# Kernel tuning notes

Hardware: AMD Instinct MI355X
Metric: run time of the kernel (lower is better)

The kernel has to match this reference:

```python
import jax, jax.numpy as jnp
import numpy as np

N, E, G = 50000, 1000000, 8
H, C, L = 4, 32, 3          # heads, per-head channels, GAT layers
HID = H * C                  # 128
NODE_D, EDGE_D, REC_D = 64, 16, 8
NEG_SLOPE = 0.2              # PyG GATConv default


def setup_inputs() -> dict:
    key = jax.random.key(0)
    ks = jax.random.split(key, 24)

    def glorot(k, shape):
        fan_in = shape[-2] if len(shape) >= 2 else shape[-1]
        return jax.random.normal(k, shape, dtype=jnp.float32) / jnp.sqrt(jnp.float32(fan_in))

    inp = {
        "x": jax.random.normal(ks[0], (N, NODE_D), dtype=jnp.float32),
        "edge_index": jax.random.randint(ks[1], (2, E), 0, N, dtype=jnp.int64),
        "edge_attr": jax.random.normal(ks[2], (E, EDGE_D), dtype=jnp.float32),
        "batch": jnp.sort(jax.random.randint(ks[3], (N,), 0, G, dtype=jnp.int64)),
        "recipe": jax.random.normal(ks[4], (G, REC_D), dtype=jnp.float32),
        # input projection + edge encoder
        "W_in": glorot(ks[5], (NODE_D + REC_D, HID)),
        "b_in": jnp.zeros((HID,), jnp.float32),
        "W_edge": glorot(ks[6], (EDGE_D, HID)),
        "b_edge": jnp.zeros((HID,), jnp.float32),
        # stacked GATConv params (PyG GATConv: lin & lin_edge have no bias)
        "lin_w": glorot(ks[7], (L, HID, HID)),
        "lin_edge_w": glorot(ks[8], (L, HID, HID)),
        "att_src": glorot(ks[9], (L, H, C)),
        "att_dst": glorot(ks[10], (L, H, C)),
        "att_edge": glorot(ks[11], (L, H, C)),
        "gat_bias": jnp.zeros((L, HID), jnp.float32),
        "W1": glorot(ks[12], (HID, HID)),
        "b1": jnp.zeros((HID,), jnp.float32),
        "W2": glorot(ks[13], (HID, 1)),
        "b2": jnp.zeros((1,), jnp.float32),
    }
    return inp


def reference(x, edge_index, edge_attr, batch, recipe,
              W_in, b_in, W_edge, b_edge,
              lin_w, lin_edge_w, att_src, att_dst, att_edge, gat_bias,
              W1, b1, W2, b2):
    src, dst = edge_index[0], edge_index[1]

    # broadcast recipe to nodes, project, relu
    h = jnp.concatenate([x, recipe[batch]], axis=1)        # [N, NODE_D+REC_D]
    h = jax.nn.relu(h @ W_in + b_in)                        # [N, HID]
    e = edge_attr @ W_edge + b_edge                         # [E, HID]

    for l in range(L):
        xl = (h @ lin_w[l]).reshape(N, H, C)                # [N,H,C]
        el = (e @ lin_edge_w[l]).reshape(E, H, C)           # [E,H,C]
        a_src = jnp.sum(xl * att_src[l], axis=-1)           # [N,H]
        a_dst = jnp.sum(xl * att_dst[l], axis=-1)           # [N,H]
        a_edge = jnp.sum(el * att_edge[l], axis=-1)         # [E,H]
        alpha = jax.nn.leaky_relu(a_src[src] + a_dst[dst] + a_edge, NEG_SLOPE)
        # segment softmax over destination nodes
        amax = jax.ops.segment_max(alpha, dst, num_segments=N)   # [N,H]
        alpha = jnp.exp(alpha - amax[dst])
        denom = jax.ops.segment_sum(alpha, dst, num_segments=N)  # [N,H]
        alpha = alpha / denom[dst]
        # weighted message scatter-add (dropout is identity in eval mode)
        msg = xl[src] * alpha[..., None]                    # [E,H,C]
        out = jax.ops.segment_sum(msg, dst, num_segments=N).reshape(N, HID) + gat_bias[l]
        h = jax.nn.relu(out)

    # global mean pool over graphs
    counts = jax.ops.segment_sum(jnp.ones((N,), h.dtype), batch, num_segments=G)
    g = jax.ops.segment_sum(h, batch, num_segments=G) / jnp.maximum(counts, 1.0)[:, None]

    return jax.nn.relu(g @ W1 + b1) @ W2 + b2               # [G,1]
```

## Files before the change

kernel.cpp:

```cpp
#include <hip/hip_runtime.h>
#include <math.h>


typedef __attribute__((ext_vector_type(8))) __bf16 bf16x8;
typedef __attribute__((ext_vector_type(4))) float f32x4;

union FragU {
  uint4 u;
  bf16x8 v;
};

__device__ __forceinline__ float lrelu(float x) { return x >= 0.f ? x : 0.2f * x; }

__device__ __forceinline__ unsigned pack_bf2(float a, float b) {
  unsigned ua = __float_as_uint(a), ub = __float_as_uint(b);
  ua += 0x7fffu + ((ua >> 16) & 1u);
  ub += 0x7fffu + ((ub >> 16) & 1u);
  return (ua >> 16) | (ub & 0xffff0000u);
}
__device__ __forceinline__ unsigned short bf_of(float a) {
  unsigned ua = __float_as_uint(a);
  ua += 0x7fffu + ((ua >> 16) & 1u);
  return (unsigned short)(ua >> 16);
}
__device__ __forceinline__ float bf_lo(unsigned u) { return __uint_as_float(u << 16); }
__device__ __forceinline__ float bf_hi(unsigned u) { return __uint_as_float(u & 0xffff0000u); }

__global__ void rank_kernel(const int* __restrict__ dst, int* __restrict__ deg,
                            int* __restrict__ rank, int E) {
  int e = blockIdx.x * 256 + threadIdx.x;
  if (e < E) rank[e] = atomicAdd(&deg[dst[e]], 1);
}

__global__ __launch_bounds__(1024) void scanA_kernel(const int* __restrict__ deg,
                                                     int* __restrict__ tmp,
                                                     int* __restrict__ bsum, int n) {
  __shared__ int wsum[16];
  int tid = threadIdx.x;
  int lane = tid & 63, wid = tid >> 6;
  int i = blockIdx.x * 1024 + tid;
  int v = (i < n) ? deg[i] : 0;
  int sv = v;
#pragma unroll
  for (int off = 1; off < 64; off <<= 1) {
    int t = __shfl_up(sv, off);
    if (lane >= off) sv += t;
  }
  if (lane == 63) wsum[wid] = sv;
  __syncthreads();
  if (wid == 0) {
    int wv = (lane < 16) ? wsum[lane] : 0;
#pragma unroll
    for (int off = 1; off < 16; off <<= 1) {
      int t = __shfl_up(wv, off);
      if (lane >= off) wv += t;
    }
    if (lane < 16) wsum[lane] = wv;
  }
  __syncthreads();
  int waveoff = (wid > 0) ? wsum[wid - 1] : 0;
  int incl = waveoff + sv;
  if (i < n) tmp[i] = incl;
  if (tid == 1023) bsum[blockIdx.x] = incl;
}

__global__ void scanB_kernel(int* __restrict__ bsum, int nb, int* __restrict__ total_out) {
  int lane = threadIdx.x;
  int v = (lane < nb) ? bsum[lane] : 0;
  int sv = v;
#pragma unroll
  for (int off = 1; off < 64; off <<= 1) {
    int t = __shfl_up(sv, off);
    if (lane >= off) sv += t;
  }
  if (lane < nb) bsum[lane] = sv - v;
  if (lane == 63) *total_out = sv;
}

__global__ __launch_bounds__(1024) void scanC_kernel(const int* __restrict__ deg,
                                                     const int* __restrict__ tmp,
                                                     const int* __restrict__ bsum,
                                                     int* __restrict__ row_ptr, int n) {
  int i = blockIdx.x * 1024 + threadIdx.x;
  if (i < n) row_ptr[i] = tmp[i] - deg[i] + bsum[blockIdx.x];
}

__global__ void perm_kernel(const int* __restrict__ dst, const int* __restrict__ srcA,
                            const int* __restrict__ rank, const int* __restrict__ row_ptr,
                            int* __restrict__ perm, int* __restrict__ src_csr, int E) {
  int e = blockIdx.x * 256 + threadIdx.x;
  if (e < E) {
    int pos = row_ptr[dst[e]] + rank[e];
    perm[pos] = e;
    src_csr[pos] = srcA[e];
  }
}

__global__ void gb_kernel(const int* __restrict__ batch, int* __restrict__ gb, int N) {
  int i = blockIdx.x * 256 + threadIdx.x;
  if (i == 0) gb[8] = N;
  if (i < N) {
    int b = batch[i];
    if (i == 0 || batch[i - 1] != b) gb[b] = i;
  }
}

__global__ void prep_params(const float* __restrict__ lin_edge_w,
                            const float* __restrict__ att_edge,
                            const float* __restrict__ W_edge,
                            const float* __restrict__ b_edge,
                            float* __restrict__ Mc) {
  __shared__ float WE[128][12];
  int t = threadIdx.x;
  for (int idx = t; idx < 128 * 12; idx += 256) {
    int k = idx / 12, j = idx - k * 12;
    int l = j >> 2, h = j & 3;
    float s = 0.f;
    for (int c = 0; c < 32; ++c)
      s += lin_edge_w[((size_t)l * 128 + k) * 128 + h * 32 + c] * att_edge[(l * 4 + h) * 32 + c];
    WE[k][j] = s;
  }
  __syncthreads();
  for (int idx = t; idx < 16 * 12; idx += 256) {
    int i = idx / 12, j = idx - i * 12;
    float s = 0.f;
    for (int k = 0; k < 128; ++k) s += W_edge[i * 128 + k] * WE[k][j];
    Mc[idx] = s;
  }
  if (t < 12) {
    float s = 0.f;
    for (int k = 0; k < 128; ++k) s += b_edge[k] * WE[k][t];
    Mc[192 + t] = s;
  }
}

__global__ __launch_bounds__(256) void prep_w_kernel(const float* __restrict__ lin_w,
                                                     unsigned short* __restrict__ wt_hi,
                                                     unsigned short* __restrict__ wt_lo) {
  __shared__ float tile[128][18];
  int l = blockIdx.x >> 3;
  int n0 = (blockIdx.x & 7) * 16;
  const float* W = lin_w + (size_t)l * 16384;
  unsigned short* hi = wt_hi + (size_t)l * 16384;
  unsigned short* lo = wt_lo + (size_t)l * 16384;
  int t = threadIdx.x;
  for (int idx = t; idx < 2048; idx += 256) {
    int k = idx >> 4, j = idx & 15;
    tile[k][j] = W[k * 128 + n0 + j];
  }
  __syncthreads();
  int r = t >> 4;
  int k0 = (t & 15) * 8;
  unsigned short hbuf[8], lbuf[8];
#pragma unroll
  for (int u = 0; u < 8; ++u) {
    float w = tile[k0 + u][r];
    unsigned short hb = bf_of(w);
    float hf = __uint_as_float((unsigned)hb << 16);
    hbuf[u] = hb;
    lbuf[u] = bf_of(w - hf);
  }
  size_t base = (size_t)(n0 + r) * 128 + k0;
  *(uint4*)(hi + base) = *(uint4*)hbuf;
  *(uint4*)(lo + base) = *(uint4*)lbuf;
}

__global__ void edge_build_kernel(const int* __restrict__ perm,
                                  const float* __restrict__ edge_attr,
                                  const float* __restrict__ Mc,
                                  unsigned short* __restrict__ a_edge_csr,
                                  int E) {
  __shared__ float M[16][12];
  __shared__ float cv[12];
  int t = threadIdx.x;
  if (t < 192) M[t / 12][t % 12] = Mc[t];
  if (t < 12) cv[t] = Mc[192 + t];
  __syncthreads();
  int i = blockIdx.x * 256 + t;
  if (i >= E) return;
  int e = perm[i];
  const float4* p = (const float4*)(edge_attr + (size_t)e * 16);
  float4 v0 = p[0], v1 = p[1], v2 = p[2], v3 = p[3];
  float ea[16] = {v0.x, v0.y, v0.z, v0.w, v1.x, v1.y, v1.z, v1.w,
                  v2.x, v2.y, v2.z, v2.w, v3.x, v3.y, v3.z, v3.w};
  float a[12];
#pragma unroll
  for (int j = 0; j < 12; ++j) {
    float s = cv[j];
#pragma unroll
    for (int k = 0; k < 16; ++k) s += ea[k] * M[k][j];
    a[j] = s;
  }
#pragma unroll
  for (int l = 0; l < 3; ++l) {
    uint2 o;
    o.x = pack_bf2(a[l * 4 + 0], a[l * 4 + 1]);
    o.y = pack_bf2(a[l * 4 + 2], a[l * 4 + 3]);
    *(uint2*)(a_edge_csr + ((size_t)l * E + i) * 4) = o;
  }
}

__global__ __launch_bounds__(256) void proj_kernel(const float* __restrict__ x,
                                                   const float* __restrict__ recipe,
                                                   const int* __restrict__ batch,
                                                   const float* __restrict__ W_in,
                                                   const float* __restrict__ b_in,
                                                   float* __restrict__ h, int N) {
  __shared__ float Wc[72][128];
  __shared__ float Ac[64][72];
  int t = threadIdx.x;
  int tx = t & 31, ty = t >> 5;
  int row0 = blockIdx.x * 64;
  for (int idx = t; idx < 2304; idx += 256) {
    int k = idx >> 5, c4 = idx & 31;
    *(float4*)&Wc[k][c4 * 4] = *(const float4*)(W_in + (size_t)k * 128 + c4 * 4);
  }
  for (int idx = t; idx < 1024; idx += 256) {
    int r = idx >> 4, c4 = idx & 15;
    int row = row0 + r;
    float4 v = make_float4(0.f, 0.f, 0.f, 0.f);
    if (row < N) v = *(const float4*)(x + (size_t)row * 64 + c4 * 4);
    *(float4*)&Ac[r][c4 * 4] = v;
  }
  for (int idx = t; idx < 128; idx += 256) {
    int r = idx >> 1, c4 = idx & 1;
    int row = row0 + r;
    float4 v = make_float4(0.f, 0.f, 0.f, 0.f);
    if (row < N) v = *(const float4*)(recipe + (size_t)batch[row] * 8 + c4 * 4);
    *(float4*)&Ac[r][64 + c4 * 4] = v;
  }
  __syncthreads();
  float4 bias = *(const float4*)(b_in + tx * 4);
  float4 acc[8];
#pragma unroll
  for (int s = 0; s < 8; ++s) acc[s] = bias;
  for (int k4 = 0; k4 < 18; ++k4) {
    float4 w0 = *(float4*)&Wc[k4 * 4 + 0][tx * 4];
    float4 w1 = *(float4*)&Wc[k4 * 4 + 1][tx * 4];
    float4 w2 = *(float4*)&Wc[k4 * 4 + 2][tx * 4];
    float4 w3 = *(float4*)&Wc[k4 * 4 + 3][tx * 4];
#pragma unroll
    for (int s = 0; s < 8; ++s) {
      float4 av = *(float4*)&Ac[ty + 8 * s][k4 * 4];
      acc[s].x += av.x * w0.x + av.y * w1.x + av.z * w2.x + av.w * w3.x;
      acc[s].y += av.x * w0.y + av.y * w1.y + av.z * w2.y + av.w * w3.y;
      acc[s].z += av.x * w0.z + av.y * w1.z + av.z * w2.z + av.w * w3.z;
      acc[s].w += av.x * w0.w + av.y * w1.w + av.z * w2.w + av.w * w3.w;
    }
  }
#pragma unroll
  for (int s = 0; s < 8; ++s) {
    int row = row0 + ty + 8 * s;
    if (row < N) {
      float4 o = acc[s];
      o.x = fmaxf(o.x, 0.f); o.y = fmaxf(o.y, 0.f);
      o.z = fmaxf(o.z, 0.f); o.w = fmaxf(o.w, 0.f);
      *(float4*)(h + (size_t)row * 128 + tx * 4) = o;
    }
  }
}

__global__ __launch_bounds__(256) void gemm_mfma_kernel(
    const float* __restrict__ A, const unsigned short* __restrict__ wt_hi,
    const unsigned short* __restrict__ wt_lo,
    const float* __restrict__ att_s, const float* __restrict__ att_d,
    unsigned short* __restrict__ Cb, float* __restrict__ a_src,
    float* __restrict__ a_dst, int M) {
  int t = threadIdx.x;
  int lane = t & 63, w = t >> 6;
  int c = lane & 15, q = lane >> 4;
  int m0 = blockIdx.x * 64 + w * 16;
  int rowA = m0 + c;
  bool rowok = rowA < M;

  f32x4 acc[8];
#pragma unroll
  for (int n = 0; n < 8; ++n) acc[n] = 0.f;

#pragma unroll
  for (int kk = 0; kk < 128; kk += 32) {
    float4 fa0 = make_float4(0.f, 0.f, 0.f, 0.f), fa1 = fa0;
    if (rowok) {
      const float* ap = A + (size_t)rowA * 128 + kk + 8 * q;
      fa0 = *(const float4*)ap;
      fa1 = *(const float4*)(ap + 4);
    }
    FragU af;
    af.u.x = pack_bf2(fa0.x, fa0.y);
    af.u.y = pack_bf2(fa0.z, fa0.w);
    af.u.z = pack_bf2(fa1.x, fa1.y);
    af.u.w = pack_bf2(fa1.z, fa1.w);
    const unsigned short* bhp = wt_hi + (size_t)c * 128 + kk + 8 * q;
    const unsigned short* blp = wt_lo + (size_t)c * 128 + kk + 8 * q;
#pragma unroll
    for (int n = 0; n < 8; ++n) {
      FragU bh, bl;
      bh.u = *(const uint4*)(bhp + n * 2048);
      bl.u = *(const uint4*)(blp + n * 2048);
      acc[n] = __builtin_amdgcn_mfma_f32_16x16x32_bf16(af.v, bh.v, acc[n], 0, 0, 0);
      acc[n] = __builtin_amdgcn_mfma_f32_16x16x32_bf16(af.v, bl.v, acc[n], 0, 0, 0);
    }
  }

  float asr[4][2], adr[4][2];
#pragma unroll
  for (int hh = 0; hh < 4; ++hh) {
    asr[hh][0] = att_s[32 * hh + c];
    asr[hh][1] = att_s[32 * hh + 16 + c];
    adr[hh][0] = att_d[32 * hh + c];
    adr[hh][1] = att_d[32 * hh + 16 + c];
  }
#pragma unroll
  for (int i = 0; i < 4; ++i) {
    int row = m0 + 4 * q + i;
    bool ok = row < M;
    if (ok) {
      size_t base = (size_t)row * 128;
#pragma unroll
      for (int n = 0; n < 8; ++n) Cb[base + n * 16 + c] = bf_of(acc[n][i]);
    }
#pragma unroll
    for (int hh = 0; hh < 4; ++hh) {
      float ps = acc[2 * hh][i] * asr[hh][0] + acc[2 * hh + 1][i] * asr[hh][1];
      float pd = acc[2 * hh][i] * adr[hh][0] + acc[2 * hh + 1][i] * adr[hh][1];
#pragma unroll
      for (int off = 1; off < 16; off <<= 1) {
        ps += __shfl_xor(ps, off);
        pd += __shfl_xor(pd, off);
      }
      if (ok && c == hh) {
        a_src[(size_t)row * 4 + hh] = ps;
        a_dst[(size_t)row * 4 + hh] = pd;
      }
    }
  }
}

__global__ __launch_bounds__(256) void node_kernel(const int* __restrict__ row_ptr,
                                                   const int* __restrict__ src_csr,
                                                   const float* __restrict__ a_src,
                                                   const float* __restrict__ a_dst,
                                                   const unsigned short* __restrict__ aep,
                                                   const unsigned short* __restrict__ xlb,
                                                   const float* __restrict__ bias,
                                                   float* __restrict__ h_out, int N) {
  int lane = threadIdx.x & 63;
  int g = lane >> 3;
  int t = lane & 7;
  int h = t >> 1;
  int n = blockIdx.x * 4 + (threadIdx.x >> 6);
  if (n >= N) return;
  int s = row_ptr[n], e = row_ptr[n + 1];

  const float* bp = bias + t * 16;
  float* op = h_out + (size_t)n * 128 + t * 16;
  if (e <= s) {
    if (g == 0) {
#pragma unroll
      for (int q = 0; q < 4; ++q) {
        float4 b = *(const float4*)(bp + q * 4);
        float4 o = make_float4(fmaxf(b.x, 0.f), fmaxf(b.y, 0.f), fmaxf(b.z, 0.f), fmaxf(b.w, 0.f));
        *(float4*)(op + q * 4) = o;
      }
    }
    return;
  }

  float ad = a_dst[(size_t)n * 4 + h];
  const unsigned* aepu = (const unsigned*)aep;
  int hw = h >> 1;
  int hb = h & 1;

  float den = 0.f;
  float num[16];
#pragma unroll
  for (int c = 0; c < 16; ++c) num[c] = 0.f;

  for (int i = s + g; i < e; i += 8) {
    int sc = src_csr[i];
    float as = a_src[(size_t)sc * 4 + h];
    unsigned uae = aepu[(size_t)i * 2 + hw];
    float ae = hb ? bf_hi(uae) : bf_lo(uae);
    const uint4* xp = (const uint4*)(xlb + (size_t)sc * 128 + t * 16);
    uint4 u0 = xp[0], u1 = xp[1];
    float a = lrelu(as + ad + ae);
    float w = __expf(fminf(a, 80.f));
    den += w;
    num[0]  += w * bf_lo(u0.x); num[1]  += w * bf_hi(u0.x);
    num[2]  += w * bf_lo(u0.y); num[3]  += w * bf_hi(u0.y);
    num[4]  += w * bf_lo(u0.z); num[5]  += w * bf_hi(u0.z);
    num[6]  += w * bf_lo(u0.w); num[7]  += w * bf_hi(u0.w);
    num[8]  += w * bf_lo(u1.x); num[9]  += w * bf_hi(u1.x);
    num[10] += w * bf_lo(u1.y); num[11] += w * bf_hi(u1.y);
    num[12] += w * bf_lo(u1.z); num[13] += w * bf_hi(u1.z);
    num[14] += w * bf_lo(u1.w); num[15] += w * bf_hi(u1.w);
  }

#pragma unroll
  for (int off = 8; off < 64; off <<= 1) {
    den += __shfl_xor(den, off);
#pragma unroll
    for (int c = 0; c < 16; ++c) num[c] += __shfl_xor(num[c], off);
  }

  if (g == 0) {
    float rh = 1.f / den;
#pragma unroll
    for (int q = 0; q < 4; ++q) {
      float4 b = *(const float4*)(bp + q * 4);
      float4 o;
      o.x = fmaxf(num[q * 4 + 0] * rh + b.x, 0.f);
      o.y = fmaxf(num[q * 4 + 1] * rh + b.y, 0.f);
      o.z = fmaxf(num[q * 4 + 2] * rh + b.z, 0.f);
      o.w = fmaxf(num[q * 4 + 3] * rh + b.w, 0.f);
      *(float4*)(op + q * 4) = o;
    }
  }
}

__global__ __launch_bounds__(256) void pool_kernel(const float* __restrict__ h,
                                                   const int* __restrict__ gb,
                                                   float* __restrict__ g_sum, int N) {
  __shared__ int st[9];
  __shared__ float red[8][132];
  int t = threadIdx.x;
  if (t < 9) {
    int m = 0x7fffffff;
    for (int j = t; j < 9; ++j) m = min(m, gb[j]);
    st[t] = min(m, N);
  }
  __syncthreads();
  int g = blockIdx.x >> 5;
  int chunk = blockIdx.x & 31;
  int gs = st[g], ge = st[g + 1];
  int rows = ge - gs;
  int c4 = t & 31, sub = t >> 5;
  float ax = 0.f, ay = 0.f, az = 0.f, aw = 0.f;
  if (rows > 0) {
    int clen = (rows + 31) >> 5;
    int cs = gs + chunk * clen;
    int ce = min(cs + clen, ge);
    for (int r = cs + sub; r < ce; r += 8) {
      float4 v = *(const float4*)(h + (size_t)r * 128 + c4 * 4);
      ax += v.x; ay += v.y; az += v.z; aw += v.w;
    }
  }
  red[sub][c4 * 4 + 0] = ax;
  red[sub][c4 * 4 + 1] = ay;
  red[sub][c4 * 4 + 2] = az;
  red[sub][c4 * 4 + 3] = aw;
  __syncthreads();
  if (t < 128 && rows > 0) {
    float s = 0.f;
#pragma unroll
    for (int u = 0; u < 8; ++u) s += red[u][t];
    atomicAdd(&g_sum[(size_t)g * 128 + t], s);
  }
}

__global__ void head_kernel(const float* __restrict__ g_sum, const int* __restrict__ gb,
                            const float* __restrict__ W1, const float* __restrict__ b1,
                            const float* __restrict__ W2, const float* __restrict__ b2,
                            float* __restrict__ out, int N) {
  __shared__ float g[8][128];
  __shared__ float t1[8][128];
  __shared__ int st[9];
  int t = threadIdx.x;
  if (t < 9) {
    int m = 0x7fffffff;
    for (int j = t; j < 9; ++j) m = min(m, gb[j]);
    st[t] = min(m, N);
  }
  __syncthreads();
  for (int idx = t; idx < 1024; idx += 256) {
    int gi = idx >> 7, ch = idx & 127;
    float cnt = (float)(st[gi + 1] - st[gi]);
    g[gi][ch] = g_sum[idx] / fmaxf(cnt, 1.f);
  }
  __syncthreads();
  for (int idx = t; idx < 1024; idx += 256) {
    int gi = idx >> 7, j = idx & 127;
    float a = b1[j];
    for (int k = 0; k < 128; ++k) a += g[gi][k] * W1[(size_t)k * 128 + j];
    t1[gi][j] = fmaxf(a, 0.f);
  }
  __syncthreads();
  if (t < 8) {
    float a = b2[0];
    for (int j = 0; j < 128; ++j) a += t1[t][j] * W2[j];
    out[t] = a;
  }
}

extern "C" void kernel_launch(void* const* d_in, const int* in_sizes, int n_in,
                              void* d_out, int out_size, void* d_ws, size_t ws_size,
                              hipStream_t stream) {
  const float* x         = (const float*)d_in[0];
  const int*   edge_idx  = (const int*)d_in[1];
  const float* edge_attr = (const float*)d_in[2];
  const int*   batch     = (const int*)d_in[3];
  const float* recipe    = (const float*)d_in[4];
  const float* W_in      = (const float*)d_in[5];
  const float* b_in      = (const float*)d_in[6];
  const float* W_edge    = (const float*)d_in[7];
  const float* b_edge    = (const float*)d_in[8];
  const float* lin_w     = (const float*)d_in[9];
  const float* lin_edge_w= (const float*)d_in[10];
  const float* att_src   = (const float*)d_in[11];
  const float* att_dst   = (const float*)d_in[12];
  const float* att_edge  = (const float*)d_in[13];
  const float* gat_bias  = (const float*)d_in[14];
  const float* W1        = (const float*)d_in[15];
  const float* b1        = (const float*)d_in[16];
  const float* W2        = (const float*)d_in[17];
  const float* b2p       = (const float*)d_in[18];

  const int N = in_sizes[3];
  const int E = in_sizes[1] / 2;
  const int* src = edge_idx;
  const int* dst = edge_idx + E;

  char* ws = (char*)d_ws;
  size_t off = 0;
  auto alloc = [&](size_t bytes) -> void* {
    void* p = ws + off;
    off += (bytes + 255) & ~(size_t)255;
    return p;
  };
  float* hA         = (float*)alloc((size_t)N * 128 * 4);
  float* hB         = (float*)alloc((size_t)N * 128 * 4);
  unsigned short* xlb = (unsigned short*)alloc((size_t)N * 128 * 2);
  float* a_srcA     = (float*)alloc((size_t)N * 4 * 4);
  float* a_dstA     = (float*)alloc((size_t)N * 4 * 4);
  unsigned short* a_edge_csr = (unsigned short*)alloc((size_t)3 * E * 4 * 2);
  int*   src_csr    = (int*)alloc((size_t)E * 4);
  int*   rank       = (int*)alloc((size_t)E * 4);
  int*   perm       = (int*)alloc((size_t)E * 4);
  int*   row_ptr    = (int*)alloc((size_t)(N + 1) * 4);
  int*   deg        = (int*)alloc((size_t)N * 4);
  int*   scan_tmp   = (int*)alloc((size_t)N * 4);
  int*   bsum       = (int*)alloc(64 * 4);
  float* Mc         = (float*)alloc(204 * 4);
  unsigned short* wt_hi = (unsigned short*)alloc((size_t)3 * 16384 * 2);
  unsigned short* wt_lo = (unsigned short*)alloc((size_t)3 * 16384 * 2);
  float* g_sum      = (float*)alloc(8 * 128 * 4);
  int*   gb         = (int*)alloc(9 * 4);
  (void)ws_size; (void)n_in; (void)out_size;

  const int eb = (E + 255) / 256;
  const int rowtiles = (N + 63) / 64;
  const int nb = (N + 1023) / 1024;

  hipMemsetAsync(deg, 0, (size_t)N * 4, stream);
  hipMemsetAsync(g_sum, 0, 8 * 128 * 4, stream);
  hipMemsetAsync(gb, 0x7f, 9 * 4, stream);

  rank_kernel<<<eb, 256, 0, stream>>>(dst, deg, rank, E);
  scanA_kernel<<<nb, 1024, 0, stream>>>(deg, scan_tmp, bsum, N);
  scanB_kernel<<<1, 64, 0, stream>>>(bsum, nb, row_ptr + N);
  scanC_kernel<<<nb, 1024, 0, stream>>>(deg, scan_tmp, bsum, row_ptr, N);
  perm_kernel<<<eb, 256, 0, stream>>>(dst, src, rank, row_ptr, perm, src_csr, E);
  gb_kernel<<<(N + 255) / 256, 256, 0, stream>>>(batch, gb, N);
  prep_params<<<1, 256, 0, stream>>>(lin_edge_w, att_edge, W_edge, b_edge, Mc);
  prep_w_kernel<<<24, 256, 0, stream>>>(lin_w, wt_hi, wt_lo);
  edge_build_kernel<<<eb, 256, 0, stream>>>(perm, edge_attr, Mc, a_edge_csr, E);
  proj_kernel<<<rowtiles, 256, 0, stream>>>(x, recipe, batch, W_in, b_in, hA, N);

  float* hcur = hA;
  float* hnxt = hB;
  for (int l = 0; l < 3; ++l) {
    gemm_mfma_kernel<<<rowtiles, 256, 0, stream>>>(hcur,
                                                   wt_hi + (size_t)l * 16384,
                                                   wt_lo + (size_t)l * 16384,
                                                   att_src + (size_t)l * 128,
                                                   att_dst + (size_t)l * 128,
                                                   xlb, a_srcA, a_dstA, N);
    node_kernel<<<(N + 3) / 4, 256, 0, stream>>>(row_ptr, src_csr, a_srcA, a_dstA,
                                                 a_edge_csr + (size_t)l * E * 4, xlb,
                                                 gat_bias + (size_t)l * 128, hnxt, N);
    float* tmp = hcur; hcur = hnxt; hnxt = tmp;
  }

  pool_kernel<<<256, 256, 0, stream>>>(hcur, gb, g_sum, N);
  head_kernel<<<1, 256, 0, stream>>>(g_sum, gb, W1, b1, W2, b2p, (float*)d_out, N);
}
```

Before: 448.3 us.

## Merge small setup kernels, pad degree counters, use bf16 union conversion

Folds the tiny scanB and gb kernels into scanA/scanC, and merges the two parameter-prep kernels into one launch, cutting the number of kernel launches. Pads each per-node degree counter to its own 64-byte slot so the atomics in rank_kernel no longer contend on shared cache lines, at the cost of a 16x larger memset and strided reads in the scan. The node kernel's bf16 unpacking is rewritten as a loop over a union of __bf16 values and left to the compiler, which may emit different conversion code.

```diff
diff --git a/kernel.cpp b/kernel.cpp
--- a/kernel.cpp
+++ b/kernel.cpp
@@ -8,6 +8,11 @@
 union FragU {
   uint4 u;
   bf16x8 v;
+};
+
+union XU {
+  uint4 u[2];
+  __bf16 b[16];
 };
 
 __device__ __forceinline__ float lrelu(float x) { return x >= 0.f ? x : 0.2f * x; }
@@ -29,17 +34,24 @@
 __global__ void rank_kernel(const int* __restrict__ dst, int* __restrict__ deg,
                             int* __restrict__ rank, int E) {
   int e = blockIdx.x * 256 + threadIdx.x;
-  if (e < E) rank[e] = atomicAdd(&deg[dst[e]], 1);
+  if (e < E) rank[e] = atomicAdd(&deg[(size_t)dst[e] * 16], 1);
 }
 
 __global__ __launch_bounds__(1024) void scanA_kernel(const int* __restrict__ deg,
+                                                     const int* __restrict__ batch,
                                                      int* __restrict__ tmp,
-                                                     int* __restrict__ bsum, int n) {
+                                                     int* __restrict__ bsum,
+                                                     int* __restrict__ gb, int n) {
   __shared__ int wsum[16];
   int tid = threadIdx.x;
   int lane = tid & 63, wid = tid >> 6;
   int i = blockIdx.x * 1024 + tid;
-  int v = (i < n) ? deg[i] : 0;
+  if (i == 0) gb[8] = n;
+  if (i < n) {
+    int b = batch[i];
+    if (i == 0 || batch[i - 1] != b) gb[b] = i;
+  }
+  int v = (i < n) ? deg[(size_t)i * 16] : 0;
   int sv = v;
 #pragma unroll
   for (int off = 1; off < 64; off <<= 1) {
@@ -64,25 +76,27 @@
   if (tid == 1023) bsum[blockIdx.x] = incl;
 }
 
-__global__ void scanB_kernel(int* __restrict__ bsum, int nb, int* __restrict__ total_out) {
-  int lane = threadIdx.x;
-  int v = (lane < nb) ? bsum[lane] : 0;
-  int sv = v;
-#pragma unroll
-  for (int off = 1; off < 64; off <<= 1) {
-    int t = __shfl_up(sv, off);
-    if (lane >= off) sv += t;
-  }
-  if (lane < nb) bsum[lane] = sv - v;
-  if (lane == 63) *total_out = sv;
-}
-
 __global__ __launch_bounds__(1024) void scanC_kernel(const int* __restrict__ deg,
                                                      const int* __restrict__ tmp,
-                                                     const int* __restrict__ bsum,
+                                                     const int* __restrict__ bsum, int nb,
                                                      int* __restrict__ row_ptr, int n) {
-  int i = blockIdx.x * 1024 + threadIdx.x;
-  if (i < n) row_ptr[i] = tmp[i] - deg[i] + bsum[blockIdx.x];
+  __shared__ int soff[2];
+  int tid = threadIdx.x;
+  if (tid < 64) {
+    int v = (tid < nb) ? bsum[tid] : 0;
+    int sv = v;
+#pragma unroll
+    for (int off = 1; off < 64; off <<= 1) {
+      int t = __shfl_up(sv, off);
+      if (tid >= off) sv += t;
+    }
+    if (tid == blockIdx.x) soff[0] = sv - v;
+    if (tid == 63) soff[1] = sv;
+  }
+  __syncthreads();
+  int i = blockIdx.x * 1024 + tid;
+  if (i < n) row_ptr[i] = tmp[i] - deg[(size_t)i * 16] + soff[0];
+  if (blockIdx.x == 0 && tid == 0) row_ptr[n] = soff[1];
 }
 
 __global__ void perm_kernel(const int* __restrict__ dst, const int* __restrict__ srcA,
@@ -96,73 +110,65 @@
   }
 }
 
-__global__ void gb_kernel(const int* __restrict__ batch, int* __restrict__ gb, int N) {
-  int i = blockIdx.x * 256 + threadIdx.x;
-  if (i == 0) gb[8] = N;
-  if (i < N) {
-    int b = batch[i];
-    if (i == 0 || batch[i - 1] != b) gb[b] = i;
-  }
-}
-
-__global__ void prep_params(const float* __restrict__ lin_edge_w,
-                            const float* __restrict__ att_edge,
-                            const float* __restrict__ W_edge,
-                            const float* __restrict__ b_edge,
-                            float* __restrict__ Mc) {
-  __shared__ float WE[128][12];
+__global__ __launch_bounds__(256) void prep_wp_kernel(const float* __restrict__ lin_w,
+                                                      unsigned short* __restrict__ wt_hi,
+                                                      unsigned short* __restrict__ wt_lo,
+                                                      const float* __restrict__ lin_edge_w,
+                                                      const float* __restrict__ att_edge,
+                                                      const float* __restrict__ W_edge,
+                                                      const float* __restrict__ b_edge,
+                                                      float* __restrict__ Mc) {
+  __shared__ float shmem[128 * 18];
   int t = threadIdx.x;
-  for (int idx = t; idx < 128 * 12; idx += 256) {
-    int k = idx / 12, j = idx - k * 12;
-    int l = j >> 2, h = j & 3;
-    float s = 0.f;
-    for (int c = 0; c < 32; ++c)
-      s += lin_edge_w[((size_t)l * 128 + k) * 128 + h * 32 + c] * att_edge[(l * 4 + h) * 32 + c];
-    WE[k][j] = s;
-  }
-  __syncthreads();
-  for (int idx = t; idx < 16 * 12; idx += 256) {
-    int i = idx / 12, j = idx - i * 12;
-    float s = 0.f;
-    for (int k = 0; k < 128; ++k) s += W_edge[i * 128 + k] * WE[k][j];
-    Mc[idx] = s;
-  }
-  if (t < 12) {
-    float s = 0.f;
-    for (int k = 0; k < 128; ++k) s += b_edge[k] * WE[k][t];
-    Mc[192 + t] = s;
-  }
-}
-
-__global__ __launch_bounds__(256) void prep_w_kernel(const float* __restrict__ lin_w,
-                                                     unsigned short* __restrict__ wt_hi,
-                                                     unsigned short* __restrict__ wt_lo) {
-  __shared__ float tile[128][18];
-  int l = blockIdx.x >> 3;
-  int n0 = (blockIdx.x & 7) * 16;
-  const float* W = lin_w + (size_t)l * 16384;
-  unsigned short* hi = wt_hi + (size_t)l * 16384;
-  unsigned short* lo = wt_lo + (size_t)l * 16384;
-  int t = threadIdx.x;
-  for (int idx = t; idx < 2048; idx += 256) {
-    int k = idx >> 4, j = idx & 15;
-    tile[k][j] = W[k * 128 + n0 + j];
-  }
-  __syncthreads();
-  int r = t >> 4;
-  int k0 = (t & 15) * 8;
-  unsigned short hbuf[8], lbuf[8];
-#pragma unroll
-  for (int u = 0; u < 8; ++u) {
-    float w = tile[k0 + u][r];
-    unsigned short hb = bf_of(w);
-    float hf = __uint_as_float((unsigned)hb << 16);
-    hbuf[u] = hb;
-    lbuf[u] = bf_of(w - hf);
-  }
-  size_t base = (size_t)(n0 + r) * 128 + k0;
-  *(uint4*)(hi + base) = *(uint4*)hbuf;
-  *(uint4*)(lo + base) = *(uint4*)lbuf;
+  if (blockIdx.x < 24) {
+    float(*tile)[18] = (float(*)[18])shmem;
+    int l = blockIdx.x >> 3;
+    int n0 = (blockIdx.x & 7) * 16;
+    const float* W = lin_w + (size_t)l * 16384;
+    unsigned short* hi = wt_hi + (size_t)l * 16384;
+    unsigned short* lo = wt_lo + (size_t)l * 16384;
+    for (int idx = t; idx < 2048; idx += 256) {
+      int k = idx >> 4, j = idx & 15;
+      tile[k][j] = W[k * 128 + n0 + j];
+    }
+    __syncthreads();
+    int r = t >> 4;
+    int k0 = (t & 15) * 8;
+    unsigned short hbuf[8], lbuf[8];
+#pragma unroll
+    for (int u = 0; u < 8; ++u) {
+      float w = tile[k0 + u][r];
+      unsigned short hb = bf_of(w);
+      float hf = __uint_as_float((unsigned)hb << 16);
+      hbuf[u] = hb;
+      lbuf[u] = bf_of(w - hf);
+    }
+    size_t base = (size_t)(n0 + r) * 128 + k0;
+    *(uint4*)(hi + base) = *(uint4*)hbuf;
+    *(uint4*)(lo + base) = *(uint4*)lbuf;
+  } else {
+    float(*WE)[12] = (float(*)[12])shmem;
+    for (int idx = t; idx < 128 * 12; idx += 256) {
+      int k = idx / 12, j = idx - k * 12;
+      int l = j >> 2, h = j & 3;
+      float s = 0.f;
+      for (int c = 0; c < 32; ++c)
+        s += lin_edge_w[((size_t)l * 128 + k) * 128 + h * 32 + c] * att_edge[(l * 4 + h) * 32 + c];
+      WE[k][j] = s;
+    }
+    __syncthreads();
+    for (int idx = t; idx < 16 * 12; idx += 256) {
+      int i = idx / 12, j = idx - i * 12;
+      float s = 0.f;
+      for (int k = 0; k < 128; ++k) s += W_edge[i * 128 + k] * WE[k][j];
+      Mc[idx] = s;
+    }
+    if (t < 12) {
+      float s = 0.f;
+      for (int k = 0; k < 128; ++k) s += b_edge[k] * WE[k][t];
+      Mc[192 + t] = s;
+    }
+  }
 }
 
 __global__ void edge_build_kernel(const int* __restrict__ perm,
@@ -382,18 +388,14 @@
     unsigned uae = aepu[(size_t)i * 2 + hw];
     float ae = hb ? bf_hi(uae) : bf_lo(uae);
     const uint4* xp = (const uint4*)(xlb + (size_t)sc * 128 + t * 16);
-    uint4 u0 = xp[0], u1 = xp[1];
+    XU xu;
+    xu.u[0] = xp[0];
+    xu.u[1] = xp[1];
     float a = lrelu(as + ad + ae);
     float w = __expf(fminf(a, 80.f));
     den += w;
-    num[0]  += w * bf_lo(u0.x); num[1]  += w * bf_hi(u0.x);
-    num[2]  += w * bf_lo(u0.y); num[3]  += w * bf_hi(u0.y);
-    num[4]  += w * bf_lo(u0.z); num[5]  += w * bf_hi(u0.z);
-    num[6]  += w * bf_lo(u0.w); num[7]  += w * bf_hi(u0.w);
-    num[8]  += w * bf_lo(u1.x); num[9]  += w * bf_hi(u1.x);
-    num[10] += w * bf_lo(u1.y); num[11] += w * bf_hi(u1.y);
-    num[12] += w * bf_lo(u1.z); num[13] += w * bf_hi(u1.z);
-    num[14] += w * bf_lo(u1.w); num[15] += w * bf_hi(u1.w);
+#pragma unroll
+    for (int c = 0; c < 16; ++c) num[c] += w * (float)xu.b[c];
   }
 
 #pragma unroll
@@ -537,7 +539,7 @@
   int*   rank       = (int*)alloc((size_t)E * 4);
   int*   perm       = (int*)alloc((size_t)E * 4);
   int*   row_ptr    = (int*)alloc((size_t)(N + 1) * 4);
-  int*   deg        = (int*)alloc((size_t)N * 4);
+  int*   deg        = (int*)alloc((size_t)N * 16 * 4);
   int*   scan_tmp   = (int*)alloc((size_t)N * 4);
   int*   bsum       = (int*)alloc(64 * 4);
   float* Mc         = (float*)alloc(204 * 4);
@@ -551,18 +553,16 @@
   const int rowtiles = (N + 63) / 64;
   const int nb = (N + 1023) / 1024;
 
-  hipMemsetAsync(deg, 0, (size_t)N * 4, stream);
+  hipMemsetAsync(deg, 0, (size_t)N * 16 * 4, stream);
   hipMemsetAsync(g_sum, 0, 8 * 128 * 4, stream);
   hipMemsetAsync(gb, 0x7f, 9 * 4, stream);
 
   rank_kernel<<<eb, 256, 0, stream>>>(dst, deg, rank, E);
-  scanA_kernel<<<nb, 1024, 0, stream>>>(deg, scan_tmp, bsum, N);
-  scanB_kernel<<<1, 64, 0, stream>>>(bsum, nb, row_ptr + N);
-  scanC_kernel<<<nb, 1024, 0, stream>>>(deg, scan_tmp, bsum, row_ptr, N);
+  scanA_kernel<<<nb, 1024, 0, stream>>>(deg, batch, scan_tmp, bsum, gb, N);
+  scanC_kernel<<<nb, 1024, 0, stream>>>(deg, scan_tmp, bsum, nb, row_ptr, N);
   perm_kernel<<<eb, 256, 0, stream>>>(dst, src, rank, row_ptr, perm, src_csr, E);
-  gb_kernel<<<(N + 255) / 256, 256, 0, stream>>>(batch, gb, N);
-  prep_params<<<1, 256, 0, stream>>>(lin_edge_w, att_edge, W_edge, b_edge, Mc);
-  prep_w_kernel<<<24, 256, 0, stream>>>(lin_w, wt_hi, wt_lo);
+  prep_wp_kernel<<<25, 256, 0, stream>>>(lin_w, wt_hi, wt_lo,
+                                         lin_edge_w, att_edge, W_edge, b_edge, Mc);
   edge_build_kernel<<<eb, 256, 0, stream>>>(perm, edge_attr, Mc, a_edge_csr, E);
   proj_kernel<<<rowtiles, 256, 0, stream>>>(x, recipe, batch, W_in, b_in, hA, N);
 
```

Result: faster. 438.1 us (-2.3%).
